# Kernel tuning notes

Hardware: AMD Instinct MI355X
Metric: run time of the kernel (lower is better)

The kernel has to match this reference:

```python
import jax, jax.numpy as jnp
import numpy as np

D_MODEL = 1024
N_HEADS = 16
HEAD = D_MODEL // N_HEADS
SEQ_THRESH = 64
EPS = 1e-12  # F.normalize eps


def setup_inputs() -> dict:
    key = jax.random.key(0)
    ks = jax.random.split(key, 12)
    B, S = 2, 2048
    scale_init = float(np.log2(SEQ_THRESH ** 2 - SEQ_THRESH))
    return {
        "query": jax.random.normal(ks[0], (B, S, D_MODEL), dtype=jnp.float32),
        "key": jax.random.normal(ks[1], (B, S, D_MODEL), dtype=jnp.float32),
        "value": jax.random.normal(ks[2], (B, S, D_MODEL), dtype=jnp.float32),
        "mask": jax.random.randint(ks[3], (B, S), 0, 2, dtype=jnp.int32),
        "Wq": jax.random.normal(ks[4], (D_MODEL, D_MODEL), dtype=jnp.float32) * (1.0 / np.sqrt(D_MODEL)),
        "bq": jnp.zeros((D_MODEL,), dtype=jnp.float32),
        "Wk": jax.random.normal(ks[5], (D_MODEL, D_MODEL), dtype=jnp.float32) * (1.0 / np.sqrt(D_MODEL)),
        "bk": jnp.zeros((D_MODEL,), dtype=jnp.float32),
        "Wv": jax.random.normal(ks[6], (D_MODEL, D_MODEL), dtype=jnp.float32) * (1.0 / np.sqrt(D_MODEL)),
        "bv": jnp.zeros((D_MODEL,), dtype=jnp.float32),
        "Wo": jax.random.normal(ks[7], (D_MODEL, D_MODEL), dtype=jnp.float32) * (1.0 / np.sqrt(D_MODEL)),
        "bo": jnp.zeros((D_MODEL,), dtype=jnp.float32),
        "scale": jnp.asarray(scale_init, dtype=jnp.float32),
    }


def _split_heads(x):
    B, S, _ = x.shape
    return x.reshape(B, S, N_HEADS, HEAD).transpose(0, 2, 1, 3)  # [B,H,S,hd]


def _center_normalize(x):
    x = x - jnp.mean(x, axis=-1, keepdims=True)
    norm = jnp.linalg.norm(x, axis=-1, keepdims=True)
    return x / jnp.maximum(norm, EPS)


def reference(query, key, value, mask, Wq, bq, Wk, bk, Wv, bv, Wo, bo, scale):
    B, Sq, _ = query.shape
    Q = _split_heads(query @ Wq.T + bq)
    K = _split_heads(key @ Wk.T + bk)
    V = _split_heads(value @ Wv.T + bv)
    Q = _center_normalize(Q)
    K = _center_normalize(K)
    scores = scale * jnp.einsum("bhqd,bhkd->bhqk", Q, K)
    scores = jnp.where(mask[:, None, None, :] == 0, jnp.float32(-1e9), scores)
    attn = jax.nn.softmax(scores, axis=-1)  # [B,H,Sq,Sk]
    ctx = jnp.einsum("bhqk,bhkd->bhqd", attn, V)
    ctx = ctx.transpose(0, 2, 1, 3).reshape(B, Sq, D_MODEL)
    ctx = ctx @ Wo.T + bo
    return (ctx, attn)
```

## Files before the change

kernel.cpp:

```cpp
#include <hip/hip_runtime.h>
#include <math.h>

#define DM   1024
#define NH   16
#define HD   64
#define BATCH 2
#define SEQ  2048
#define MR   (BATCH*SEQ)

typedef __attribute__((ext_vector_type(8))) short bf16x8;
typedef __attribute__((ext_vector_type(4))) float f32x4;

__device__ __forceinline__ unsigned short f2bf(float x) {
    unsigned u = __builtin_bit_cast(unsigned, x);
    u = (u + 0x7FFFu + ((u >> 16) & 1u)) >> 16;
    return (unsigned short)u;
}
__device__ __forceinline__ float bf2f(unsigned short s) {
    unsigned u = ((unsigned)s) << 16;
    return __builtin_bit_cast(float, u);
}
__device__ __forceinline__ uint4 packhi8(const float* f, unsigned short* h) {
#pragma unroll
    for (int k = 0; k < 8; ++k) h[k] = f2bf(f[k]);
    uint4 u;
    u.x = (unsigned)h[0] | ((unsigned)h[1] << 16);
    u.y = (unsigned)h[2] | ((unsigned)h[3] << 16);
    u.z = (unsigned)h[4] | ((unsigned)h[5] << 16);
    u.w = (unsigned)h[6] | ((unsigned)h[7] << 16);
    return u;
}

__global__ __launch_bounds__(256) void convert_split(
    const float* __restrict__ src, unsigned short* __restrict__ hi,
    unsigned short* __restrict__ lo, int n4)
{
    int i = blockIdx.x * 256 + threadIdx.x;
    if (i >= n4) return;
    float4 v = ((const float4*)src)[i];
    float f[4] = {v.x, v.y, v.z, v.w};
    unsigned short h[4], l[4];
#pragma unroll
    for (int k = 0; k < 4; ++k) {
        h[k] = f2bf(f[k]);
        l[k] = f2bf(f[k] - bf2f(h[k]));
    }
    ((ushort4*)hi)[i] = make_ushort4(h[0], h[1], h[2], h[3]);
    ((ushort4*)lo)[i] = make_ushort4(l[0], l[1], l[2], l[3]);
}

__global__ __launch_bounds__(256) void convert_single(
    const float* __restrict__ src, unsigned short* __restrict__ dst, int n4)
{
    int i = blockIdx.x * 256 + threadIdx.x;
    if (i >= n4) return;
    float4 v = ((const float4*)src)[i];
    ((ushort4*)dst)[i] = make_ushort4(f2bf(v.x), f2bf(v.y), f2bf(v.z), f2bf(v.w));
}

template<int MODE>
__global__ __launch_bounds__(256) void proj_gemm(
    const void* __restrict__ Aptr,
    const unsigned short* __restrict__ Bhi, const unsigned short* __restrict__ Blo,
    const float* __restrict__ bias,
    void* __restrict__ out0, unsigned short* __restrict__ out1)
{
    __shared__ __align__(16) short As[2][64][40];
    __shared__ __align__(16) short Bs[2][128][40];

    const int tid  = threadIdx.x;
    const int wave = tid >> 6, lane = tid & 63;
    const int quad = lane >> 4, lr = lane & 15;
    const int wy = wave >> 1, wx = wave & 1;
    const int m0 = blockIdx.x * 64, n0 = blockIdx.y * 128;

    f32x4 acc[2][4];
#pragma unroll
    for (int i = 0; i < 2; ++i)
#pragma unroll
        for (int j = 0; j < 4; ++j) acc[i][j] = (f32x4){0.f, 0.f, 0.f, 0.f};

    const int arow = tid >> 2, aseg = tid & 3;
    const int brow = tid >> 1, bseg = tid & 1;

    for (int k0 = 0; k0 < DM; k0 += 32) {
        __syncthreads();
        if (MODE == 2) {
            const unsigned short* A = (const unsigned short*)Aptr;
            *(uint4*)&As[0][arow][aseg * 8] =
                *(const uint4*)&A[(size_t)(m0 + arow) * DM + k0 + aseg * 8];
        } else {
            const float* A = (const float*)Aptr;
            const float* ap = &A[(size_t)(m0 + arow) * DM + k0 + aseg * 8];
            float4 v0 = *(const float4*)ap;
            float4 v1 = *(const float4*)(ap + 4);
            float f[8] = {v0.x, v0.y, v0.z, v0.w, v1.x, v1.y, v1.z, v1.w};
            unsigned short h[8];
            uint4 hv = packhi8(f, h);
            *(uint4*)&As[0][arow][aseg * 8] = hv;
            if (MODE == 0) {
                float fl[8];
#pragma unroll
                for (int k = 0; k < 8; ++k) fl[k] = f[k] - bf2f(h[k]);
                unsigned short hl[8];
                uint4 lv = packhi8(fl, hl);
                *(uint4*)&As[1][arow][aseg * 8] = lv;
            }
        }
        {
            const size_t bo = (size_t)(n0 + brow) * DM + k0 + bseg * 16;
            *(uint4*)&Bs[0][brow][bseg * 16]     = *(const uint4*)&Bhi[bo];
            *(uint4*)&Bs[0][brow][bseg * 16 + 8] = *(const uint4*)&Bhi[bo + 8];
            if (MODE == 0) {
                *(uint4*)&Bs[1][brow][bseg * 16]     = *(const uint4*)&Blo[bo];
                *(uint4*)&Bs[1][brow][bseg * 16 + 8] = *(const uint4*)&Blo[bo + 8];
            }
        }
        __syncthreads();
        bf16x8 ah[2], al[2], bh[4], bl[4];
#pragma unroll
        for (int i = 0; i < 2; ++i) {
            ah[i] = *(const bf16x8*)&As[0][wy * 32 + i * 16 + lr][quad * 8];
            if (MODE == 0) al[i] = *(const bf16x8*)&As[1][wy * 32 + i * 16 + lr][quad * 8];
        }
#pragma unroll
        for (int j = 0; j < 4; ++j) {
            bh[j] = *(const bf16x8*)&Bs[0][wx * 64 + j * 16 + lr][quad * 8];
            if (MODE == 0) bl[j] = *(const bf16x8*)&Bs[1][wx * 64 + j * 16 + lr][quad * 8];
        }
#pragma unroll
        for (int i = 0; i < 2; ++i)
#pragma unroll
            for (int j = 0; j < 4; ++j) {
                acc[i][j] = __builtin_amdgcn_mfma_f32_16x16x32_bf16(ah[i], bh[j], acc[i][j], 0, 0, 0);
                if (MODE == 0) {
                    acc[i][j] = __builtin_amdgcn_mfma_f32_16x16x32_bf16(ah[i], bl[j], acc[i][j], 0, 0, 0);
                    acc[i][j] = __builtin_amdgcn_mfma_f32_16x16x32_bf16(al[i], bh[j], acc[i][j], 0, 0, 0);
                }
            }
    }

    float bj[4];
#pragma unroll
    for (int j = 0; j < 4; ++j) bj[j] = bias[n0 + wx * 64 + j * 16 + lr];

    if (MODE == 0) {
        unsigned short* Ohi = (unsigned short*)out0;
#pragma unroll
        for (int i = 0; i < 2; ++i) {
#pragma unroll
            for (int r = 0; r < 4; ++r) {
                float x[4];
#pragma unroll
                for (int j = 0; j < 4; ++j) x[j] = acc[i][j][r] + bj[j];
                float t = x[0] + x[1] + x[2] + x[3];
                t += __shfl_xor(t, 1, 16);
                t += __shfl_xor(t, 2, 16);
                t += __shfl_xor(t, 4, 16);
                t += __shfl_xor(t, 8, 16);
                const float mean = t * (1.0f / 64.0f);
                float ss = 0.f;
#pragma unroll
                for (int j = 0; j < 4; ++j) { x[j] -= mean; ss += x[j] * x[j]; }
                ss += __shfl_xor(ss, 1, 16);
                ss += __shfl_xor(ss, 2, 16);
                ss += __shfl_xor(ss, 4, 16);
                ss += __shfl_xor(ss, 8, 16);
                const float inv = 1.0f / fmaxf(sqrtf(ss), 1e-12f);
                const int row = m0 + wy * 32 + i * 16 + quad * 4 + r;
#pragma unroll
                for (int j = 0; j < 4; ++j) {
                    const float y = x[j] * inv;
                    const unsigned short hh = f2bf(y);
                    const unsigned short ll = f2bf(y - bf2f(hh));
                    const size_t o = (size_t)row * DM + n0 + wx * 64 + j * 16 + lr;
                    Ohi[o]  = hh;
                    out1[o] = ll;
                }
            }
        }
    } else if (MODE == 1) {
        unsigned short* Vg = (unsigned short*)out0;
        const int h = (n0 + wx * 64) >> 6;
#pragma unroll
        for (int i = 0; i < 2; ++i) {
            const int grow = m0 + wy * 32 + i * 16 + quad * 4;
            const int bb = grow >> 11, ss = grow & (SEQ - 1);
#pragma unroll
            for (int j = 0; j < 4; ++j) {
                const int d = j * 16 + lr;
                ushort4 pk;
                pk.x = f2bf(acc[i][j][0] + bj[j]);
                pk.y = f2bf(acc[i][j][1] + bj[j]);
                pk.z = f2bf(acc[i][j][2] + bj[j]);
                pk.w = f2bf(acc[i][j][3] + bj[j]);
                *(ushort4*)&Vg[((size_t)(bb * NH + h) * HD + d) * SEQ + ss] = pk;
            }
        }
    } else {
        float* O = (float*)out0;
#pragma unroll
        for (int i = 0; i < 2; ++i)
#pragma unroll
            for (int j = 0; j < 4; ++j)
#pragma unroll
                for (int r = 0; r < 4; ++r)
                    O[(size_t)(m0 + wy * 32 + i * 16 + quad * 4 + r) * DM +
                      n0 + wx * 64 + j * 16 + lr] = acc[i][j][r] + bj[j];
    }
}

__global__ __launch_bounds__(256) void attn_fused(
    const unsigned short* __restrict__ Qhi, const unsigned short* __restrict__ Qlo,
    const unsigned short* __restrict__ Khi, const unsigned short* __restrict__ Klo,
    const unsigned short* __restrict__ Vg,  const int* __restrict__ mask,
    const float* __restrict__ scale_p,
    float* __restrict__ attn, unsigned short* __restrict__ ctxb)
{
    __shared__ __align__(16) short KHs[64][72];
    __shared__ __align__(16) short KLs[64][72];
    __shared__ __align__(16) short Vs[64][72];
    __shared__ __align__(16) short Ps[64][72];
    __shared__ int mk[64];

    const int tid = threadIdx.x;
    const int w = tid >> 6, lane = tid & 63;
    const int quad = lane >> 4, lr = lane & 15;
    const int b = blockIdx.z, h = blockIdx.y, q0 = blockIdx.x * 64;

    const float scl = scale_p[0];
    const float s2 = scl * 1.44269504089f;
    const float c2 = -12.0f * 1.44269504089f;

    const int r0 = tid >> 3,        c0 = (tid & 7) * 8;
    const int r1 = (tid >> 3) + 32, c1 = (tid & 7) * 8;

    {
        const size_t base = ((size_t)(b * SEQ + q0)) * DM + h * HD;
        *(uint4*)&KHs[r0][c0] = *(const uint4*)&Qhi[base + (size_t)r0 * DM + c0];
        *(uint4*)&KHs[r1][c1] = *(const uint4*)&Qhi[base + (size_t)r1 * DM + c1];
        *(uint4*)&KLs[r0][c0] = *(const uint4*)&Qlo[base + (size_t)r0 * DM + c0];
        *(uint4*)&KLs[r1][c1] = *(const uint4*)&Qlo[base + (size_t)r1 * DM + c1];
    }
    __syncthreads();
    bf16x8 qh[2], ql[2];
#pragma unroll
    for (int kc = 0; kc < 2; ++kc) {
        qh[kc] = *(const bf16x8*)&KHs[w * 16 + lr][kc * 32 + quad * 8];
        ql[kc] = *(const bf16x8*)&KLs[w * 16 + lr][kc * 32 + quad * 8];
    }

    float rs[4] = {0.f, 0.f, 0.f, 0.f};

    for (int kt = 0; kt < SEQ / 64; ++kt) {
        const int kk = kt * 64;
        const size_t kb = ((size_t)(b * SEQ + kk)) * DM + h * HD;
        __syncthreads();
        *(uint4*)&KHs[r0][c0] = *(const uint4*)&Khi[kb + (size_t)r0 * DM + c0];
        *(uint4*)&KHs[r1][c1] = *(const uint4*)&Khi[kb + (size_t)r1 * DM + c1];
        *(uint4*)&KLs[r0][c0] = *(const uint4*)&Klo[kb + (size_t)r0 * DM + c0];
        *(uint4*)&KLs[r1][c1] = *(const uint4*)&Klo[kb + (size_t)r1 * DM + c1];
        if (tid < 64) mk[tid] = mask[b * SEQ + kk + tid];
        __syncthreads();
#pragma unroll
        for (int j = 0; j < 4; ++j) {
            bf16x8 bh0 = *(const bf16x8*)&KHs[j * 16 + lr][quad * 8];
            bf16x8 bh1 = *(const bf16x8*)&KHs[j * 16 + lr][32 + quad * 8];
            bf16x8 bl0 = *(const bf16x8*)&KLs[j * 16 + lr][quad * 8];
            bf16x8 bl1 = *(const bf16x8*)&KLs[j * 16 + lr][32 + quad * 8];
            f32x4 sa = (f32x4){0.f, 0.f, 0.f, 0.f};
            sa = __builtin_amdgcn_mfma_f32_16x16x32_bf16(qh[0], bh0, sa, 0, 0, 0);
            sa = __builtin_amdgcn_mfma_f32_16x16x32_bf16(ql[0], bh0, sa, 0, 0, 0);
            sa = __builtin_amdgcn_mfma_f32_16x16x32_bf16(qh[0], bl0, sa, 0, 0, 0);
            sa = __builtin_amdgcn_mfma_f32_16x16x32_bf16(qh[1], bh1, sa, 0, 0, 0);
            sa = __builtin_amdgcn_mfma_f32_16x16x32_bf16(ql[1], bh1, sa, 0, 0, 0);
            sa = __builtin_amdgcn_mfma_f32_16x16x32_bf16(qh[1], bl1, sa, 0, 0, 0);
            const float mcol = mk[j * 16 + lr] ? 1.0f : 0.0f;
#pragma unroll
            for (int r = 0; r < 4; ++r)
                rs[r] += mcol * exp2f(fmaf(sa[r], s2, c2));
        }
    }

    float rinv[4];
#pragma unroll
    for (int r = 0; r < 4; ++r) {
        float t = rs[r];
        t += __shfl_xor(t, 1, 16);
        t += __shfl_xor(t, 2, 16);
        t += __shfl_xor(t, 4, 16);
        t += __shfl_xor(t, 8, 16);
        rinv[r] = 1.0f / fmaxf(t, 1e-30f);
    }

    f32x4 acc_o[4];
#pragma unroll
    for (int dt = 0; dt < 4; ++dt) acc_o[dt] = (f32x4){0.f, 0.f, 0.f, 0.f};

    for (int kt = 0; kt < SEQ / 64; ++kt) {
        const int kk = kt * 64;
        const size_t kb = ((size_t)(b * SEQ + kk)) * DM + h * HD;
        const size_t vb = ((size_t)((b * NH + h) * HD)) * SEQ + kk;
        __syncthreads();
        *(uint4*)&KHs[r0][c0] = *(const uint4*)&Khi[kb + (size_t)r0 * DM + c0];
        *(uint4*)&KHs[r1][c1] = *(const uint4*)&Khi[kb + (size_t)r1 * DM + c1];
        *(uint4*)&KLs[r0][c0] = *(const uint4*)&Klo[kb + (size_t)r0 * DM + c0];
        *(uint4*)&KLs[r1][c1] = *(const uint4*)&Klo[kb + (size_t)r1 * DM + c1];
        *(uint4*)&Vs[r0][c0]  = *(const uint4*)&Vg[vb + (size_t)r0 * SEQ + c0];
        *(uint4*)&Vs[r1][c1]  = *(const uint4*)&Vg[vb + (size_t)r1 * SEQ + c1];
        if (tid < 64) mk[tid] = mask[b * SEQ + kk + tid];
        __syncthreads();
#pragma unroll
        for (int j = 0; j < 4; ++j) {
            bf16x8 bh0 = *(const bf16x8*)&KHs[j * 16 + lr][quad * 8];
            bf16x8 bh1 = *(const bf16x8*)&KHs[j * 16 + lr][32 + quad * 8];
            bf16x8 bl0 = *(const bf16x8*)&KLs[j * 16 + lr][quad * 8];
            bf16x8 bl1 = *(const bf16x8*)&KLs[j * 16 + lr][32 + quad * 8];
            f32x4 sa = (f32x4){0.f, 0.f, 0.f, 0.f};
            sa = __builtin_amdgcn_mfma_f32_16x16x32_bf16(qh[0], bh0, sa, 0, 0, 0);
            sa = __builtin_amdgcn_mfma_f32_16x16x32_bf16(ql[0], bh0, sa, 0, 0, 0);
            sa = __builtin_amdgcn_mfma_f32_16x16x32_bf16(qh[0], bl0, sa, 0, 0, 0);
            sa = __builtin_amdgcn_mfma_f32_16x16x32_bf16(qh[1], bh1, sa, 0, 0, 0);
            sa = __builtin_amdgcn_mfma_f32_16x16x32_bf16(ql[1], bh1, sa, 0, 0, 0);
            sa = __builtin_amdgcn_mfma_f32_16x16x32_bf16(qh[1], bl1, sa, 0, 0, 0);
            const float mcol = mk[j * 16 + lr] ? 1.0f : 0.0f;
#pragma unroll
            for (int r = 0; r < 4; ++r) {
                const float pn = mcol * exp2f(fmaf(sa[r], s2, c2)) * rinv[r];
                const int qrow = q0 + w * 16 + quad * 4 + r;
                attn[((size_t)(b * NH + h) * SEQ + qrow) * SEQ + kk + j * 16 + lr] = pn;
                Ps[w * 16 + quad * 4 + r][j * 16 + lr] = (short)f2bf(pn);
            }
        }
        bf16x8 pa0 = *(const bf16x8*)&Ps[w * 16 + lr][quad * 8];
        bf16x8 pa1 = *(const bf16x8*)&Ps[w * 16 + lr][32 + quad * 8];
#pragma unroll
        for (int dt = 0; dt < 4; ++dt) {
            bf16x8 bv0 = *(const bf16x8*)&Vs[dt * 16 + lr][quad * 8];
            bf16x8 bv1 = *(const bf16x8*)&Vs[dt * 16 + lr][32 + quad * 8];
            acc_o[dt] = __builtin_amdgcn_mfma_f32_16x16x32_bf16(pa0, bv0, acc_o[dt], 0, 0, 0);
            acc_o[dt] = __builtin_amdgcn_mfma_f32_16x16x32_bf16(pa1, bv1, acc_o[dt], 0, 0, 0);
        }
    }

#pragma unroll
    for (int dt = 0; dt < 4; ++dt)
#pragma unroll
        for (int r = 0; r < 4; ++r)
            ctxb[((size_t)(b * SEQ + q0 + w * 16 + quad * 4 + r)) * DM +
                 h * HD + dt * 16 + lr] = (unsigned short)f2bf(acc_o[dt][r]);
}

extern "C" void kernel_launch(void* const* d_in, const int* in_sizes, int n_in,
                              void* d_out, int out_size, void* d_ws, size_t ws_size,
                              hipStream_t stream)
{
    const float* query = (const float*)d_in[0];
    const float* key   = (const float*)d_in[1];
    const float* value = (const float*)d_in[2];
    const int*   mask  = (const int*)d_in[3];
    const float* Wq = (const float*)d_in[4];
    const float* bq = (const float*)d_in[5];
    const float* Wk = (const float*)d_in[6];
    const float* bk = (const float*)d_in[7];
    const float* Wv = (const float*)d_in[8];
    const float* bv = (const float*)d_in[9];
    const float* Wo = (const float*)d_in[10];
    const float* bo = (const float*)d_in[11];
    const float* scale = (const float*)d_in[12];

    float* out_ctx  = (float*)d_out;
    float* out_attn = out_ctx + (size_t)MR * DM;

    const size_t WSZ = (size_t)DM * DM;
    const size_t TSZ = (size_t)MR * DM;
    unsigned short* p = (unsigned short*)d_ws;
    unsigned short* Wq_hi = p; p += WSZ;
    unsigned short* Wq_lo = p; p += WSZ;
    unsigned short* Wk_hi = p; p += WSZ;
    unsigned short* Wk_lo = p; p += WSZ;
    unsigned short* Wv_b  = p; p += WSZ;
    unsigned short* Wo_b  = p; p += WSZ;
    unsigned short* Qn_hi = p; p += TSZ;
    unsigned short* Qn_lo = p; p += TSZ;
    unsigned short* Kn_hi = p; p += TSZ;
    unsigned short* Kn_lo = p; p += TSZ;
    unsigned short* Vg    = p; p += TSZ;
    unsigned short* ctxb  = Wq_hi;

    convert_split <<<1024, 256, 0, stream>>>(Wq, Wq_hi, Wq_lo, 262144);
    convert_split <<<1024, 256, 0, stream>>>(Wk, Wk_hi, Wk_lo, 262144);
    convert_single<<<1024, 256, 0, stream>>>(Wv, Wv_b, 262144);
    convert_single<<<1024, 256, 0, stream>>>(Wo, Wo_b, 262144);

    dim3 gg(MR / 64, DM / 128);
    proj_gemm<0><<<gg, 256, 0, stream>>>(query, Wq_hi, Wq_lo, bq, Qn_hi, Qn_lo);
    proj_gemm<0><<<gg, 256, 0, stream>>>(key,   Wk_hi, Wk_lo, bk, Kn_hi, Kn_lo);
    proj_gemm<1><<<gg, 256, 0, stream>>>(value, Wv_b, nullptr, bv, Vg, nullptr);

    attn_fused<<<dim3(SEQ / 64, NH, BATCH), 256, 0, stream>>>(
        Qn_hi, Qn_lo, Kn_hi, Kn_lo, Vg, mask, scale, out_attn, ctxb);

    proj_gemm<2><<<gg, 256, 0, stream>>>(ctxb, Wo_b, nullptr, bo, out_ctx, nullptr);
}
```

Measured before the change: 946.2 us.

## Pre-split activations to bf16 hi/lo, swizzle attention grid, fold mask into exponent

Activations are converted to bf16 hi/lo once by a separate kernel into scratch space borrowed from the attention output buffer, so the projection GEMMs load bf16 directly. This removes the repeated fp32 load and conversion that every column block of the GEMM used to perform. The attention grid is flattened and swizzled so that concurrently running blocks are spread across batch, head and query tiles, with the intent of improving K/V cache locality. The mask becomes a per-column additive offset inside exp2, which drops a multiply. In exchange there are extra conversion kernels with their own global round trips, and the scratch buffer lives inside the output until attention overwrites it.

```diff
diff --git a/kernel.cpp b/kernel.cpp
--- a/kernel.cpp
+++ b/kernel.cpp
@@ -20,16 +20,6 @@
     unsigned u = ((unsigned)s) << 16;
     return __builtin_bit_cast(float, u);
 }
-__device__ __forceinline__ uint4 packhi8(const float* f, unsigned short* h) {
-#pragma unroll
-    for (int k = 0; k < 8; ++k) h[k] = f2bf(f[k]);
-    uint4 u;
-    u.x = (unsigned)h[0] | ((unsigned)h[1] << 16);
-    u.y = (unsigned)h[2] | ((unsigned)h[3] << 16);
-    u.z = (unsigned)h[4] | ((unsigned)h[5] << 16);
-    u.w = (unsigned)h[6] | ((unsigned)h[7] << 16);
-    return u;
-}
 
 __global__ __launch_bounds__(256) void convert_split(
     const float* __restrict__ src, unsigned short* __restrict__ hi,
@@ -60,7 +50,7 @@
 
 template<int MODE>
 __global__ __launch_bounds__(256) void proj_gemm(
-    const void* __restrict__ Aptr,
+    const unsigned short* __restrict__ Ahi, const unsigned short* __restrict__ Alo,
     const unsigned short* __restrict__ Bhi, const unsigned short* __restrict__ Blo,
     const float* __restrict__ bias,
     void* __restrict__ out0, unsigned short* __restrict__ out1)
@@ -80,40 +70,24 @@
 #pragma unroll
         for (int j = 0; j < 4; ++j) acc[i][j] = (f32x4){0.f, 0.f, 0.f, 0.f};
 
-    const int arow = tid >> 2, aseg = tid & 3;
-    const int brow = tid >> 1, bseg = tid & 1;
+    const int arow = tid >> 2, aseg = (tid & 3) * 8;
+    const int brow = tid >> 1, bseg = (tid & 1) * 16;
 
     for (int k0 = 0; k0 < DM; k0 += 32) {
         __syncthreads();
-        if (MODE == 2) {
-            const unsigned short* A = (const unsigned short*)Aptr;
-            *(uint4*)&As[0][arow][aseg * 8] =
-                *(const uint4*)&A[(size_t)(m0 + arow) * DM + k0 + aseg * 8];
-        } else {
-            const float* A = (const float*)Aptr;
-            const float* ap = &A[(size_t)(m0 + arow) * DM + k0 + aseg * 8];
-            float4 v0 = *(const float4*)ap;
-            float4 v1 = *(const float4*)(ap + 4);
-            float f[8] = {v0.x, v0.y, v0.z, v0.w, v1.x, v1.y, v1.z, v1.w};
-            unsigned short h[8];
-            uint4 hv = packhi8(f, h);
-            *(uint4*)&As[0][arow][aseg * 8] = hv;
+        {
+            const size_t ao = (size_t)(m0 + arow) * DM + k0 + aseg;
+            *(uint4*)&As[0][arow][aseg] = *(const uint4*)&Ahi[ao];
+            if (MODE == 0)
+                *(uint4*)&As[1][arow][aseg] = *(const uint4*)&Alo[ao];
+        }
+        {
+            const size_t bo = (size_t)(n0 + brow) * DM + k0 + bseg;
+            *(uint4*)&Bs[0][brow][bseg]     = *(const uint4*)&Bhi[bo];
+            *(uint4*)&Bs[0][brow][bseg + 8] = *(const uint4*)&Bhi[bo + 8];
             if (MODE == 0) {
-                float fl[8];
-#pragma unroll
-                for (int k = 0; k < 8; ++k) fl[k] = f[k] - bf2f(h[k]);
-                unsigned short hl[8];
-                uint4 lv = packhi8(fl, hl);
-                *(uint4*)&As[1][arow][aseg * 8] = lv;
-            }
-        }
-        {
-            const size_t bo = (size_t)(n0 + brow) * DM + k0 + bseg * 16;
-            *(uint4*)&Bs[0][brow][bseg * 16]     = *(const uint4*)&Bhi[bo];
-            *(uint4*)&Bs[0][brow][bseg * 16 + 8] = *(const uint4*)&Bhi[bo + 8];
-            if (MODE == 0) {
-                *(uint4*)&Bs[1][brow][bseg * 16]     = *(const uint4*)&Blo[bo];
-                *(uint4*)&Bs[1][brow][bseg * 16 + 8] = *(const uint4*)&Blo[bo + 8];
+                *(uint4*)&Bs[1][brow][bseg]     = *(const uint4*)&Blo[bo];
+                *(uint4*)&Bs[1][brow][bseg + 8] = *(const uint4*)&Blo[bo + 8];
             }
         }
         __syncthreads();
@@ -221,12 +195,17 @@
     __shared__ __align__(16) short KLs[64][72];
     __shared__ __align__(16) short Vs[64][72];
     __shared__ __align__(16) short Ps[64][72];
-    __shared__ int mk[64];
+    __shared__ float mkf[64];
 
     const int tid = threadIdx.x;
     const int w = tid >> 6, lane = tid & 63;
     const int quad = lane >> 4, lr = lane & 15;
-    const int b = blockIdx.z, h = blockIdx.y, q0 = blockIdx.x * 64;
+
+    const int lin = blockIdx.x;
+    const int swz = (lin & 7) * 128 + (lin >> 3);
+    const int b  = swz >> 9;
+    const int h  = (swz >> 5) & 15;
+    const int q0 = (swz & 31) * 64;
 
     const float scl = scale_p[0];
     const float s2 = scl * 1.44269504089f;
@@ -260,7 +239,7 @@
         *(uint4*)&KHs[r1][c1] = *(const uint4*)&Khi[kb + (size_t)r1 * DM + c1];
         *(uint4*)&KLs[r0][c0] = *(const uint4*)&Klo[kb + (size_t)r0 * DM + c0];
         *(uint4*)&KLs[r1][c1] = *(const uint4*)&Klo[kb + (size_t)r1 * DM + c1];
-        if (tid < 64) mk[tid] = mask[b * SEQ + kk + tid];
+        if (tid < 64) mkf[tid] = mask[b * SEQ + kk + tid] ? c2 : -3.0e38f;
         __syncthreads();
 #pragma unroll
         for (int j = 0; j < 4; ++j) {
@@ -275,10 +254,10 @@
             sa = __builtin_amdgcn_mfma_f32_16x16x32_bf16(qh[1], bh1, sa, 0, 0, 0);
             sa = __builtin_amdgcn_mfma_f32_16x16x32_bf16(ql[1], bh1, sa, 0, 0, 0);
             sa = __builtin_amdgcn_mfma_f32_16x16x32_bf16(qh[1], bl1, sa, 0, 0, 0);
-            const float mcol = mk[j * 16 + lr] ? 1.0f : 0.0f;
+            const float mo = mkf[j * 16 + lr];
 #pragma unroll
             for (int r = 0; r < 4; ++r)
-                rs[r] += mcol * exp2f(fmaf(sa[r], s2, c2));
+                rs[r] += exp2f(fmaf(sa[r], s2, mo));
         }
     }
 
@@ -308,7 +287,7 @@
         *(uint4*)&KLs[r1][c1] = *(const uint4*)&Klo[kb + (size_t)r1 * DM + c1];
         *(uint4*)&Vs[r0][c0]  = *(const uint4*)&Vg[vb + (size_t)r0 * SEQ + c0];
         *(uint4*)&Vs[r1][c1]  = *(const uint4*)&Vg[vb + (size_t)r1 * SEQ + c1];
-        if (tid < 64) mk[tid] = mask[b * SEQ + kk + tid];
+        if (tid < 64) mkf[tid] = mask[b * SEQ + kk + tid] ? c2 : -3.0e38f;
         __syncthreads();
 #pragma unroll
         for (int j = 0; j < 4; ++j) {
@@ -323,10 +302,10 @@
             sa = __builtin_amdgcn_mfma_f32_16x16x32_bf16(qh[1], bh1, sa, 0, 0, 0);
             sa = __builtin_amdgcn_mfma_f32_16x16x32_bf16(ql[1], bh1, sa, 0, 0, 0);
             sa = __builtin_amdgcn_mfma_f32_16x16x32_bf16(qh[1], bl1, sa, 0, 0, 0);
-            const float mcol = mk[j * 16 + lr] ? 1.0f : 0.0f;
+            const float mo = mkf[j * 16 + lr];
 #pragma unroll
             for (int r = 0; r < 4; ++r) {
-                const float pn = mcol * exp2f(fmaf(sa[r], s2, c2)) * rinv[r];
+                const float pn = exp2f(fmaf(sa[r], s2, mo)) * rinv[r];
                 const int qrow = q0 + w * 16 + quad * 4 + r;
                 attn[((size_t)(b * NH + h) * SEQ + qrow) * SEQ + kk + j * 16 + lr] = pn;
                 Ps[w * 16 + quad * 4 + r][j * 16 + lr] = (short)f2bf(pn);
@@ -387,6 +366,8 @@
     unsigned short* Kn_lo = p; p += TSZ;
     unsigned short* Vg    = p; p += TSZ;
     unsigned short* ctxb  = Wq_hi;
+    unsigned short* Ahi = (unsigned short*)out_attn;
+    unsigned short* Alo = Ahi + TSZ;
 
     convert_split <<<1024, 256, 0, stream>>>(Wq, Wq_hi, Wq_lo, 262144);
     convert_split <<<1024, 256, 0, stream>>>(Wk, Wk_hi, Wk_lo, 262144);
@@ -394,12 +375,16 @@
     convert_single<<<1024, 256, 0, stream>>>(Wo, Wo_b, 262144);
 
     dim3 gg(MR / 64, DM / 128);
-    proj_gemm<0><<<gg, 256, 0, stream>>>(query, Wq_hi, Wq_lo, bq, Qn_hi, Qn_lo);
-    proj_gemm<0><<<gg, 256, 0, stream>>>(key,   Wk_hi, Wk_lo, bk, Kn_hi, Kn_lo);
-    proj_gemm<1><<<gg, 256, 0, stream>>>(value, Wv_b, nullptr, bv, Vg, nullptr);
-
-    attn_fused<<<dim3(SEQ / 64, NH, BATCH), 256, 0, stream>>>(
+
+    convert_split <<<4096, 256, 0, stream>>>(query, Ahi, Alo, (int)(TSZ / 4));
+    proj_gemm<0><<<gg, 256, 0, stream>>>(Ahi, Alo, Wq_hi, Wq_lo, bq, Qn_hi, Qn_lo);
+    convert_split <<<4096, 256, 0, stream>>>(key, Ahi, Alo, (int)(TSZ / 4));
+    proj_gemm<0><<<gg, 256, 0, stream>>>(Ahi, Alo, Wk_hi, Wk_lo, bk, Kn_hi, Kn_lo);
+    convert_single<<<4096, 256, 0, stream>>>(value, Ahi, (int)(TSZ / 4));
+    proj_gemm<1><<<gg, 256, 0, stream>>>(Ahi, nullptr, Wv_b, nullptr, bv, Vg, nullptr);
+
+    attn_fused<<<dim3(SEQ / 64 * NH * BATCH), 256, 0, stream>>>(
         Qn_hi, Qn_lo, Kn_hi, Kn_lo, Vg, mask, scale, out_attn, ctxb);
 
-    proj_gemm<2><<<gg, 256, 0, stream>>>(ctxb, Wo_b, nullptr, bo, out_ctx, nullptr);
-}
+    proj_gemm<2><<<gg, 256, 0, stream>>>(ctxb, nullptr, Wo_b, nullptr, bo, out_ctx, nullptr);
+}
```

After: 920.2 us. 2.7% less time.
